# Kernel tuning notes

Measured on AMD Instinct MI355X. Metric: run time of the kernel, lower is better.

## Reference

```python
import jax, jax.numpy as jnp
import numpy as np

COMMITMENT_COST = 0.25
NUM_EMBEDDINGS = 1024
EMBEDDING_DIM = 512  # win_size(8) * num_pellets(64)


def setup_inputs() -> dict:
    key = jax.random.key(0)
    k1, k2 = jax.random.split(key)
    inputs = jax.random.normal(k1, (64, 256, EMBEDDING_DIM), dtype=jnp.float32)
    # matches torch init: uniform_(-1/K, 1/K)
    lim = 1.0 / NUM_EMBEDDINGS
    emb_weight = jax.random.uniform(k2, (NUM_EMBEDDINGS, EMBEDDING_DIM),
                                    dtype=jnp.float32, minval=-lim, maxval=lim)
    return {"inputs": inputs, "emb_weight": emb_weight}


def reference(inputs, emb_weight):
    batch_size = inputs.shape[0]
    input_shape = inputs.shape
    flat = inputs.reshape(-1, EMBEDDING_DIM)  # [N, D]

    distances = (jnp.sum(flat * flat, axis=1, keepdims=True)
                 + jnp.sum(emb_weight * emb_weight, axis=1)
                 - 2.0 * flat @ emb_weight.T)
    encoding_indices = jnp.argmin(distances, axis=1)  # [N]

    # gather instead of one-hot matmul (same math)
    quantized = emb_weight[encoding_indices].reshape(input_shape)

    e_latent_loss = jnp.mean((jax.lax.stop_gradient(quantized) - inputs) ** 2)
    q_latent_loss = jnp.mean((quantized - jax.lax.stop_gradient(inputs)) ** 2)
    loss_vq = q_latent_loss + COMMITMENT_COST * e_latent_loss

    # straight-through estimator
    quantized = inputs + jax.lax.stop_gradient(quantized - inputs)

    encoding_indices = encoding_indices.reshape(batch_size, -1)
    return loss_vq, quantized, encoding_indices
```

## Files before the change

kernel.cpp:

```cpp
#include <hip/hip_runtime.h>
#include <cfloat>

#define NROWS  16384
#define DIM    512
#define KC     1024
#define QELEMS (NROWS * DIM)

#define NSPLIT 8
#define CHUNKS 130

typedef float  floatx4 __attribute__((ext_vector_type(4)));
typedef _Float16 half8 __attribute__((ext_vector_type(8)));
typedef _Float16 half4 __attribute__((ext_vector_type(4)));

#define KBARRIER() do { \
    asm volatile("s_waitcnt lgkmcnt(0)" ::: "memory"); \
    __builtin_amdgcn_s_barrier(); \
} while (0)

__global__ __launch_bounds__(256) void prep_kernel(const float* __restrict__ A,
                                                   const float* __restrict__ E,
                                                   float* __restrict__ xsq,
                                                   float* __restrict__ esq,
                                                   _Float16* __restrict__ ah,
                                                   _Float16* __restrict__ al,
                                                   _Float16* __restrict__ eh,
                                                   _Float16* __restrict__ el,
                                                   unsigned long long* __restrict__ packed,
                                                   float* __restrict__ out) {
    if (blockIdx.x == 0 && threadIdx.x == 0) out[0] = 0.f;
    const int wave = threadIdx.x >> 6, lane = threadIdx.x & 63;
    const bool isA = blockIdx.x < (NROWS / 4);
    const int row = (isA ? blockIdx.x : blockIdx.x - NROWS / 4) * 4 + wave;
    const float* M = isA ? A : E;
    const float scale = isA ? 2048.0f : 65536.0f;

    const float4* Mr = (const float4*)(M + (size_t)row * DIM);
    float4 va = Mr[lane];
    float4 vb = Mr[lane + 64];
    float s = 0.f;
    s += va.x*va.x + va.y*va.y + va.z*va.z + va.w*va.w;
    s += vb.x*vb.x + vb.y*vb.y + vb.z*vb.z + vb.w*vb.w;
    #pragma unroll
    for (int off = 32; off; off >>= 1) s += __shfl_down(s, off, 64);
    if (lane == 0) {
        if (isA) { xsq[row] = s; packed[row] = ~0ULL; }
        else     { esq[row] = s; }
    }

    float xa[4] = {va.x, va.y, va.z, va.w}, xb[4] = {vb.x, vb.y, vb.z, vb.w};
    half4 ha, la, hb, lb;
    #pragma unroll
    for (int e = 0; e < 4; ++e) {
        float t = xa[e] * scale;
        _Float16 h = (_Float16)t;
        ha[e] = h; la[e] = (_Float16)(t - (float)h);
        t = xb[e] * scale;
        h = (_Float16)t;
        hb[e] = h; lb[e] = (_Float16)(t - (float)h);
    }
    _Float16* hr = (isA ? ah : eh) + (size_t)row * DIM;
    _Float16* lr = (isA ? al : el) + (size_t)row * DIM;
    ((half4*)hr)[lane]      = ha;
    ((half4*)lr)[lane]      = la;
    ((half4*)hr)[lane + 64] = hb;
    ((half4*)lr)[lane + 64] = lb;
}

#define LOAD_SET(S, koff) \
    S##A0 = *(const half8*)(gA  + (koff)); \
    S##A1 = *(const half8*)(gA  + 64 * DIM + (koff)); \
    S##L0 = *(const half8*)(gAl + (koff)); \
    S##L1 = *(const half8*)(gAl + 64 * DIM + (koff)); \
    S##E0 = *(const half8*)(gE  + (koff)); \
    S##E1 = *(const half8*)(gE  + 64 * DIM + (koff)); \
    S##F0 = *(const half8*)(gEl + (koff)); \
    S##F1 = *(const half8*)(gEl + 64 * DIM + (koff));

#define STORE_SET(S, b) \
    AhT[b][cw0] = S##A0; AhT[b][cw1] = S##A1; \
    AlT[b][cw0] = S##L0; AlT[b][cw1] = S##L1; \
    EhT[b][cw0] = S##E0; EhT[b][cw1] = S##E1; \
    ElT[b][cw0] = S##F0; ElT[b][cw1] = S##F1;

#define COMPUTE(b) { \
    half8 fa[4], fbh[4], fbl[4]; \
    _Pragma("unroll") \
    for (int i = 0; i < 4; ++i) \
        fa[i] = AhT[b][qd * CHUNKS + wm * 64 + i * 16 + tx]; \
    _Pragma("unroll") \
    for (int j = 0; j < 4; ++j) { \
        fbh[j] = EhT[b][qd * CHUNKS + wn * 64 + j * 16 + tx]; \
        fbl[j] = ElT[b][qd * CHUNKS + wn * 64 + j * 16 + tx]; \
    } \
    __builtin_amdgcn_s_setprio(1); \
    _Pragma("unroll") \
    for (int i = 0; i < 4; ++i) \
        _Pragma("unroll") \
        for (int j = 0; j < 4; ++j) \
            acc[i][j] = __builtin_amdgcn_mfma_f32_16x16x32_f16(fa[i], fbh[j], acc[i][j], 0, 0, 0); \
    _Pragma("unroll") \
    for (int i = 0; i < 4; ++i) \
        _Pragma("unroll") \
        for (int j = 0; j < 4; ++j) \
            acc[i][j] = __builtin_amdgcn_mfma_f32_16x16x32_f16(fa[i], fbl[j], acc[i][j], 0, 0, 0); \
    __builtin_amdgcn_s_setprio(0); \
    _Pragma("unroll") \
    for (int i = 0; i < 4; ++i) \
        fa[i] = AlT[b][qd * CHUNKS + wm * 64 + i * 16 + tx]; \
    __builtin_amdgcn_s_setprio(1); \
    _Pragma("unroll") \
    for (int i = 0; i < 4; ++i) \
        _Pragma("unroll") \
        for (int j = 0; j < 4; ++j) \
            acc[i][j] = __builtin_amdgcn_mfma_f32_16x16x32_f16(fa[i], fbh[j], acc[i][j], 0, 0, 0); \
    __builtin_amdgcn_s_setprio(0); \
}

__global__ __launch_bounds__(256, 2) void mfma_argmin_kernel(const _Float16* __restrict__ ah,
                                                             const _Float16* __restrict__ al,
                                                             const _Float16* __restrict__ eh,
                                                             const _Float16* __restrict__ el,
                                                             const float* __restrict__ esq,
                                                             const float* __restrict__ xsq,
                                                             unsigned long long* __restrict__ packed) {
    __shared__ half8 AhT[2][4 * CHUNKS], AlT[2][4 * CHUNKS];
    __shared__ half8 EhT[2][4 * CHUNKS], ElT[2][4 * CHUNKS];
    __shared__ float redv[128][2];
    __shared__ int   redi[128][2];

    const int tid = threadIdx.x;
    const int lane = tid & 63, wave = tid >> 6;
    const int wm = wave >> 1, wn = wave & 1;
    const int tx = lane & 15, qd = lane >> 4;
    const int bm = blockIdx.x & 127, bn = blockIdx.x >> 7;
    const int m0 = bm * 128, c0 = bn * 128;

    const int srow = tid >> 2, skq = tid & 3;
    const _Float16* gA  = ah + (size_t)(m0 + srow) * DIM + skq * 8;
    const _Float16* gAl = al + (size_t)(m0 + srow) * DIM + skq * 8;
    const _Float16* gE  = eh + (size_t)(c0 + srow) * DIM + skq * 8;
    const _Float16* gEl = el + (size_t)(c0 + srow) * DIM + skq * 8;
    const int cw0 = skq * CHUNKS + srow, cw1 = cw0 + 64;

    floatx4 acc[4][4];
    #pragma unroll
    for (int i = 0; i < 4; ++i)
        #pragma unroll
        for (int j = 0; j < 4; ++j) acc[i][j] = (floatx4){0.f, 0.f, 0.f, 0.f};

    half8 pA0, pA1, pL0, pL1, pE0, pE1, pF0, pF1;
    half8 qA0, qA1, qL0, qL1, qE0, qE1, qF0, qF1;

    LOAD_SET(p, 0);
    STORE_SET(p, 0);
    LOAD_SET(q, 32);

    #pragma unroll 1
    for (int k2 = 0; k2 < 8; ++k2) {
        const int kt = k2 * 2;
        if (kt + 2 < 16) { LOAD_SET(p, (kt + 2) * 32); }
        KBARRIER();
        COMPUTE(0);
        STORE_SET(q, 1);
        if (kt + 3 < 16) { LOAD_SET(q, (kt + 3) * 32); }
        KBARRIER();
        COMPUTE(1);
        if (kt + 2 < 16) { STORE_SET(p, 0); }
    }

    float sqe_v[4];
    #pragma unroll
    for (int j = 0; j < 4; ++j) sqe_v[j] = esq[c0 + wn * 64 + j * 16 + tx];
    #pragma unroll
    for (int i = 0; i < 4; ++i) {
        #pragma unroll
        for (int r = 0; r < 4; ++r) {
            int rl = wm * 64 + i * 16 + qd * 4 + r;
            float sx = xsq[m0 + rl];
            float bvv = FLT_MAX; int bii = 0x7fffffff;
            #pragma unroll
            for (int j = 0; j < 4; ++j) {
                float S = sx + sqe_v[j];
                float s = S - acc[i][j][r] * (1.0f / 67108864.0f);
                int c = c0 + wn * 64 + j * 16 + tx;
                if (s < bvv || (s == bvv && c < bii)) { bvv = s; bii = c; }
            }
            #pragma unroll
            for (int md = 1; md < 16; md <<= 1) {
                float ov = __shfl_xor(bvv, md, 64);
                int   oc = __shfl_xor(bii, md, 64);
                if (ov < bvv || (ov == bvv && oc < bii)) { bvv = ov; bii = oc; }
            }
            if (tx == 0) { redv[rl][wn] = bvv; redi[rl][wn] = bii; }
        }
    }
    __syncthreads();
    if (tid < 128) {
        float v0 = redv[tid][0], v1 = redv[tid][1];
        int   i0 = redi[tid][0], i1 = redi[tid][1];
        float v = (v1 < v0) ? v1 : v0;
        int   ix = (v1 < v0) ? i1 : i0;
        unsigned long long pk = ((unsigned long long)__float_as_uint(v) << 32)
                              | (unsigned int)ix;
        atomicMin(&packed[m0 + tid], pk);
    }
}

__global__ __launch_bounds__(256) void finalize_kernel(const float* __restrict__ E,
                                                       const unsigned long long* __restrict__ packed,
                                                       float* __restrict__ out) {
    float* q = out + 1;
    float* idxF = out + 1 + QELEMS;
    const int tid = threadIdx.x;
    const int r0 = blockIdx.x * 16;

    __shared__ int sidx[16];
    if (tid < 64) {
        float sc = 0.f;
        if (tid < 16) {
            unsigned long long pk = packed[r0 + tid];
            int idx = (int)(unsigned int)(pk & 0xFFFFFFFFull);
            sc = __uint_as_float((unsigned int)(pk >> 32));
            sidx[tid] = idx;
            idxF[r0 + tid] = (float)idx;
        }
        #pragma unroll
        for (int off = 8; off; off >>= 1) sc += __shfl_down(sc, off, 16);
        if (tid == 0) atomicAdd(out, sc * (1.25f / (float)QELEMS));
    }
    __syncthreads();

    #pragma unroll 4
    for (int it = 0; it < 8; ++it) {
        int flat = it * 256 + tid;
        int row = flat >> 7;
        int d4  = (flat & 127) * 4;
        int idx = sidx[row];
        float4 e = *(const float4*)(E + (size_t)idx * DIM + d4);
        *(float4*)(q + (size_t)(r0 + row) * DIM + d4) = e;
    }
}

extern "C" void kernel_launch(void* const* d_in, const int* in_sizes, int n_in,
                              void* d_out, int out_size, void* d_ws, size_t ws_size,
                              hipStream_t stream) {
    const float* A = (const float*)d_in[0];
    const float* E = (const float*)d_in[1];
    float* out = (float*)d_out;

    unsigned long long* packed = (unsigned long long*)d_ws;
    float*    esq  = (float*)(packed + NROWS);
    float*    xsq  = esq + KC;
    _Float16* eh   = (_Float16*)(xsq + NROWS);
    _Float16* el   = eh + (size_t)KC * DIM;
    _Float16* ah   = el + (size_t)KC * DIM;
    _Float16* al   = ah + (size_t)NROWS * DIM;

    prep_kernel<<<NROWS / 4 + KC / 4, 256, 0, stream>>>(A, E, xsq, esq, ah, al, eh, el, packed, out);
    mfma_argmin_kernel<<<(NROWS / 128) * NSPLIT, 256, 0, stream>>>(
        ah, al, eh, el, esq, xsq, packed);
    finalize_kernel<<<NROWS / 16, 256, 0, stream>>>(E, packed, out);
}
```

Baseline: 176.9 us.

## Single-buffer LDS tiles and one register prefetch set to raise occupancy to 3 blocks

Replaces the double-buffered LDS tiles and two register prefetch sets with one LDS buffer and one register staging set. Each k-step now computes, barriers, stores the next tile and issues the load for the tile after that. Launch bounds rise from 2 to 3 blocks per CU, since LDS and register use shrink. In exchange each iteration adds a barrier between compute and store, which serializes LDS writes with MFMA work.

```diff
diff --git a/kernel.cpp b/kernel.cpp
--- a/kernel.cpp
+++ b/kernel.cpp
@@ -77,21 +77,21 @@
     S##F0 = *(const half8*)(gEl + (koff)); \
     S##F1 = *(const half8*)(gEl + 64 * DIM + (koff));
 
-#define STORE_SET(S, b) \
-    AhT[b][cw0] = S##A0; AhT[b][cw1] = S##A1; \
-    AlT[b][cw0] = S##L0; AlT[b][cw1] = S##L1; \
-    EhT[b][cw0] = S##E0; EhT[b][cw1] = S##E1; \
-    ElT[b][cw0] = S##F0; ElT[b][cw1] = S##F1;
-
-#define COMPUTE(b) { \
+#define STORE_SET(S) \
+    AhT[cw0] = S##A0; AhT[cw1] = S##A1; \
+    AlT[cw0] = S##L0; AlT[cw1] = S##L1; \
+    EhT[cw0] = S##E0; EhT[cw1] = S##E1; \
+    ElT[cw0] = S##F0; ElT[cw1] = S##F1;
+
+#define COMPUTE() { \
     half8 fa[4], fbh[4], fbl[4]; \
     _Pragma("unroll") \
     for (int i = 0; i < 4; ++i) \
-        fa[i] = AhT[b][qd * CHUNKS + wm * 64 + i * 16 + tx]; \
+        fa[i] = AhT[qd * CHUNKS + wm * 64 + i * 16 + tx]; \
     _Pragma("unroll") \
     for (int j = 0; j < 4; ++j) { \
-        fbh[j] = EhT[b][qd * CHUNKS + wn * 64 + j * 16 + tx]; \
-        fbl[j] = ElT[b][qd * CHUNKS + wn * 64 + j * 16 + tx]; \
+        fbh[j] = EhT[qd * CHUNKS + wn * 64 + j * 16 + tx]; \
+        fbl[j] = ElT[qd * CHUNKS + wn * 64 + j * 16 + tx]; \
     } \
     __builtin_amdgcn_s_setprio(1); \
     _Pragma("unroll") \
@@ -107,7 +107,7 @@
     __builtin_amdgcn_s_setprio(0); \
     _Pragma("unroll") \
     for (int i = 0; i < 4; ++i) \
-        fa[i] = AlT[b][qd * CHUNKS + wm * 64 + i * 16 + tx]; \
+        fa[i] = AlT[qd * CHUNKS + wm * 64 + i * 16 + tx]; \
     __builtin_amdgcn_s_setprio(1); \
     _Pragma("unroll") \
     for (int i = 0; i < 4; ++i) \
@@ -117,15 +117,15 @@
     __builtin_amdgcn_s_setprio(0); \
 }
 
-__global__ __launch_bounds__(256, 2) void mfma_argmin_kernel(const _Float16* __restrict__ ah,
+__global__ __launch_bounds__(256, 3) void mfma_argmin_kernel(const _Float16* __restrict__ ah,
                                                              const _Float16* __restrict__ al,
                                                              const _Float16* __restrict__ eh,
                                                              const _Float16* __restrict__ el,
                                                              const float* __restrict__ esq,
                                                              const float* __restrict__ xsq,
                                                              unsigned long long* __restrict__ packed) {
-    __shared__ half8 AhT[2][4 * CHUNKS], AlT[2][4 * CHUNKS];
-    __shared__ half8 EhT[2][4 * CHUNKS], ElT[2][4 * CHUNKS];
+    __shared__ half8 AhT[4 * CHUNKS], AlT[4 * CHUNKS];
+    __shared__ half8 EhT[4 * CHUNKS], ElT[4 * CHUNKS];
     __shared__ float redv[128][2];
     __shared__ int   redi[128][2];
 
@@ -149,24 +149,21 @@
         #pragma unroll
         for (int j = 0; j < 4; ++j) acc[i][j] = (floatx4){0.f, 0.f, 0.f, 0.f};
 
-    half8 pA0, pA1, pL0, pL1, pE0, pE1, pF0, pF1;
-    half8 qA0, qA1, qL0, qL1, qE0, qE1, qF0, qF1;
-
-    LOAD_SET(p, 0);
-    STORE_SET(p, 0);
-    LOAD_SET(q, 32);
+    half8 sA0, sA1, sL0, sL1, sE0, sE1, sF0, sF1;
+
+    LOAD_SET(s, 0);
+    STORE_SET(s);
+    LOAD_SET(s, 32);
 
     #pragma unroll 1
-    for (int k2 = 0; k2 < 8; ++k2) {
-        const int kt = k2 * 2;
-        if (kt + 2 < 16) { LOAD_SET(p, (kt + 2) * 32); }
+    for (int kt = 0; kt < 16; ++kt) {
         KBARRIER();
-        COMPUTE(0);
-        STORE_SET(q, 1);
-        if (kt + 3 < 16) { LOAD_SET(q, (kt + 3) * 32); }
-        KBARRIER();
-        COMPUTE(1);
-        if (kt + 2 < 16) { STORE_SET(p, 0); }
+        COMPUTE();
+        if (kt < 15) {
+            KBARRIER();
+            STORE_SET(s);
+            if (kt < 14) { LOAD_SET(s, (kt + 2) * 32); }
+        }
     }
 
     float sqe_v[4];
```

Measured after the change: 174.3 us. Within noise of the previous version (-1.5%).
